# Optimization experiments

Hardware: AMD Instinct MI355X
Metric: run time of the kernel (lower is better)

The kernel has to match this reference:

```python
import jax, jax.numpy as jnp
import numpy as np

ENC_DIM, DEC_DIM, ATT_DIM = 2048, 512, 512

def setup_inputs() -> dict:
    key = jax.random.key(0)
    ks = jax.random.split(key, 8)
    s_enc = 1.0 / np.sqrt(ENC_DIM)
    s_dec = 1.0 / np.sqrt(DEC_DIM)
    s_att = 1.0 / np.sqrt(ATT_DIM)
    return {
        "encoder_out": jax.random.normal(ks[0], (256, 196, ENC_DIM), jnp.float32),
        "decoder_hidden": jax.random.normal(ks[1], (256, DEC_DIM), jnp.float32),
        "W_enc": jax.random.uniform(ks[2], (ENC_DIM, ATT_DIM), jnp.float32, -s_enc, s_enc),
        "b_enc": jax.random.uniform(ks[3], (ATT_DIM,), jnp.float32, -s_enc, s_enc),
        "W_dec": jax.random.uniform(ks[4], (DEC_DIM, ATT_DIM), jnp.float32, -s_dec, s_dec),
        "b_dec": jax.random.uniform(ks[5], (ATT_DIM,), jnp.float32, -s_dec, s_dec),
        "W_att": jax.random.uniform(ks[6], (ATT_DIM, 1), jnp.float32, -s_att, s_att),
        "b_att": jax.random.uniform(ks[7], (1,), jnp.float32, -s_att, s_att),
    }

def reference(encoder_out, decoder_hidden, W_enc, b_enc, W_dec, b_dec, W_att, b_att):
    # att1: (B, P, A); att2: (B, 1, A)
    att1 = jnp.einsum('bpe,ea->bpa', encoder_out, W_enc) + b_enc
    att2 = (decoder_hidden @ W_dec + b_dec)[:, None, :]
    # scalar score per pixel: (B, P)
    e = (jax.nn.relu(att1 + att2) @ W_att)[..., 0] + b_att[0]
    alpha = jax.nn.softmax(e, axis=-1)  # softmax over pixels
    z = jnp.einsum('bpe,bp->be', encoder_out, alpha)
    return (z, alpha)
```

## Files before the change

### kernel.cpp

```cpp
#include <hip/hip_runtime.h>
#include <hip/hip_bf16.h>

#define ENC_DIM 2048
#define DEC_DIM 512
#define ATT_DIM 512
#define NB 256
#define NP 196
#define M_TOT (NB * NP)
#define BM 128
#define BK 32
#define NSTEP (ENC_DIM / BK)

typedef __attribute__((ext_vector_type(8))) short short8;
typedef __attribute__((ext_vector_type(4))) float f32x4;

__device__ __forceinline__ short8 cvt8v(f32x4 x, f32x4 y) {
    union { short8 v; __hip_bfloat16 h[8]; } u;
    u.h[0] = __float2bfloat16(x[0]);
    u.h[1] = __float2bfloat16(x[1]);
    u.h[2] = __float2bfloat16(x[2]);
    u.h[3] = __float2bfloat16(x[3]);
    u.h[4] = __float2bfloat16(y[0]);
    u.h[5] = __float2bfloat16(y[1]);
    u.h[6] = __float2bfloat16(y[2]);
    u.h[7] = __float2bfloat16(y[3]);
    return u.v;
}

__global__ __launch_bounds__(256) void prep_kernel(const float* __restrict__ W,
                                                   __hip_bfloat16* __restrict__ Btt,
                                                   const float* __restrict__ dec,
                                                   const float* __restrict__ W_dec,
                                                   const float* __restrict__ b_dec,
                                                   const float* __restrict__ b_enc,
                                                   float* __restrict__ att2f) {
    __shared__ float ds[DEC_DIM];
    if (blockIdx.x < 512) {
        const int gid = blockIdx.x * 256 + threadIdx.x;
        const int s   = gid >> 11;
        const int u   = gid & 2047;
        const int fr  = u >> 6;
        const int kg  = (u >> 4) & 3;
        const int l15 = u & 15;
        const int col = fr * 16 + l15;
        const int k0  = s * 32 + kg * 8;
        union { short8 v; __hip_bfloat16 h[8]; } x;
        #pragma unroll
        for (int i = 0; i < 8; ++i)
            x.h[i] = __float2bfloat16(W[(size_t)(k0 + i) * ATT_DIM + col]);
        *(short8*)((short*)Btt + (size_t)gid * 8) = x.v;
    } else {
        const int b = blockIdx.x - 512;
        const int t = threadIdx.x;
        ds[t]       = dec[(size_t)b * DEC_DIM + t];
        ds[t + 256] = dec[(size_t)b * DEC_DIM + t + 256];
        __syncthreads();
        #pragma unroll
        for (int j = 0; j < 2; ++j) {
            const int n = t + j * 256;
            float s = 0.f;
            #pragma unroll 8
            for (int k = 0; k < DEC_DIM; ++k)
                s += ds[k] * W_dec[(size_t)k * ATT_DIM + n];
            att2f[(size_t)b * ATT_DIM + n] = s + b_dec[n] + b_enc[n];
        }
    }
}

__global__ __launch_bounds__(512, 2) void e_kernel(const float* __restrict__ enc,
                                                   const short* __restrict__ Btt,
                                                   const float* __restrict__ att2f,
                                                   const float* __restrict__ W_att,
                                                   float* __restrict__ e_part) {
    __shared__ __attribute__((aligned(16))) short As[2][4096];
    __shared__ float ebuf[8][128];

    const int tid  = threadIdx.x;
    const int lane = tid & 63;
    const int wv   = tid >> 6;
    const int l15  = lane & 15;
    const int kg   = lane >> 4;

    const int bid = blockIdx.x;
    const int g   = bid >> 4;
    const int r   = bid & 15;
    const int nh  = r >> 3;
    const int mt  = g * 8 + (r & 7);
    const int M0  = mt * BM;
    const int N0  = nh * 256;

    const int srow = tid >> 2;
    const int sc   = tid & 3;
    const float* asrc = enc + (size_t)(M0 + srow) * ENC_DIM + sc * 8;
    const int awr = (srow >> 4) * 512 + sc * 128 + (srow & 15) * 8;

    const short* pBb = Btt + (nh * 16 + wv * 2) * 512 + kg * 128 + l15 * 8;

    f32x4 acc[8][2];
    #pragma unroll
    for (int i = 0; i < 8; ++i) {
        acc[i][0] = (f32x4){0.f, 0.f, 0.f, 0.f};
        acc[i][1] = (f32x4){0.f, 0.f, 0.f, 0.f};
    }

#define MFMA_STEP(BUF, B0, B1)                                                           \
    {                                                                                    \
        const short* Ab = &As[BUF][0];                                                   \
        _Pragma("unroll")                                                                \
        for (int mf = 0; mf < 8; ++mf) {                                                 \
            const short8 a = *(const short8*)&Ab[mf * 512 + lane * 8];                   \
            acc[mf][0] = __builtin_amdgcn_mfma_f32_16x16x32_bf16(a, B0, acc[mf][0], 0, 0, 0); \
            acc[mf][1] = __builtin_amdgcn_mfma_f32_16x16x32_bf16(a, B1, acc[mf][1], 0, 0, 0); \
        }                                                                                \
    }

    {
        f32x4 lo = *(const f32x4*)asrc;
        f32x4 hi = *(const f32x4*)(asrc + 4);
        *(short8*)&As[0][awr] = cvt8v(lo, hi);
    }
    f32x4 avPa = *(const f32x4*)(asrc + BK);
    f32x4 avPb = *(const f32x4*)(asrc + BK + 4);
    short8 c0 = *(const short8*)(pBb);
    short8 c1 = *(const short8*)(pBb + 512);
    short8 n0, n1;
    asm volatile("s_waitcnt lgkmcnt(0)" ::: "memory");
    __builtin_amdgcn_s_barrier();

    for (int s = 0; s < NSTEP; s += 2) {
        {
            const short* p1 = pBb + (size_t)(s + 1) * 16384;
            n0 = *(const short8*)(p1);
            n1 = *(const short8*)(p1 + 512);
            f32x4 avNa = *(const f32x4*)(asrc + (size_t)((s + 2) & 63) * BK);
            f32x4 avNb = *(const f32x4*)(asrc + (size_t)((s + 2) & 63) * BK + 4);
            __builtin_amdgcn_sched_barrier(0);
            __builtin_amdgcn_s_setprio(1);
            MFMA_STEP(0, c0, c1)
            __builtin_amdgcn_s_setprio(0);
            *(short8*)&As[1][awr] = cvt8v(avPa, avPb);
            avPa = avNa; avPb = avNb;
            asm volatile("s_waitcnt lgkmcnt(0)" ::: "memory");
            __builtin_amdgcn_s_barrier();
        }
        {
            const short* p2 = pBb + (size_t)((s + 2) & 63) * 16384;
            c0 = *(const short8*)(p2);
            c1 = *(const short8*)(p2 + 512);
            f32x4 avNa = *(const f32x4*)(asrc + (size_t)((s + 3) & 63) * BK);
            f32x4 avNb = *(const f32x4*)(asrc + (size_t)((s + 3) & 63) * BK + 4);
            __builtin_amdgcn_sched_barrier(0);
            __builtin_amdgcn_s_setprio(1);
            MFMA_STEP(1, n0, n1)
            __builtin_amdgcn_s_setprio(0);
            *(short8*)&As[0][awr] = cvt8v(avPa, avPb);
            avPa = avNa; avPb = avNb;
            asm volatile("s_waitcnt lgkmcnt(0)" ::: "memory");
            __builtin_amdgcn_s_barrier();
        }
    }
#undef MFMA_STEP

    float wat[2];
    wat[0] = W_att[N0 + wv * 32 + l15];
    wat[1] = W_att[N0 + wv * 32 + 16 + l15];

    #pragma unroll
    for (int mf = 0; mf < 8; ++mf) {
        #pragma unroll
        for (int rr = 0; rr < 4; ++rr) {
            const int ml = mf * 16 + kg * 4 + rr;
            const int bb = (M0 + ml) / NP;
            const float* arow2 = att2f + (size_t)bb * ATT_DIM + N0 + wv * 32 + l15;
            float sv = fmaxf(acc[mf][0][rr] + arow2[0], 0.f) * wat[0] +
                       fmaxf(acc[mf][1][rr] + arow2[16], 0.f) * wat[1];
            sv += __shfl_xor(sv, 1);
            sv += __shfl_xor(sv, 2);
            sv += __shfl_xor(sv, 4);
            sv += __shfl_xor(sv, 8);
            if (l15 == 0) ebuf[wv][ml] = sv;
        }
    }
    __syncthreads();
    if (tid < 128) {
        float sv = 0.f;
        #pragma unroll
        for (int w = 0; w < 8; ++w) sv += ebuf[w][tid];
        e_part[(size_t)nh * M_TOT + M0 + tid] = sv;
    }
}

__global__ __launch_bounds__(256) void z_kernel(const float* __restrict__ enc,
                                                const float* __restrict__ e_part,
                                                float* __restrict__ z,
                                                float* __restrict__ alpha) {
    const int b  = blockIdx.x;
    const int cb = blockIdx.y;
    const int t  = threadIdx.x;
    __shared__ float al[NP];
    __shared__ float red[4];

    float ev = -1e30f;
    if (t < NP)
        ev = e_part[(size_t)b * NP + t] + e_part[(size_t)M_TOT + b * NP + t];
    float m = ev;
    #pragma unroll
    for (int o = 32; o > 0; o >>= 1) m = fmaxf(m, __shfl_xor(m, o));
    if ((t & 63) == 0) red[t >> 6] = m;
    __syncthreads();
    m = fmaxf(fmaxf(red[0], red[1]), fmaxf(red[2], red[3]));
    __syncthreads();
    float ex = (t < NP) ? __expf(ev - m) : 0.f;
    float s = ex;
    #pragma unroll
    for (int o = 32; o > 0; o >>= 1) s += __shfl_xor(s, o);
    if ((t & 63) == 0) red[t >> 6] = s;
    __syncthreads();
    s = red[0] + red[1] + red[2] + red[3];
    const float a = ex * (1.0f / s);
    if (t < NP) {
        al[t] = a;
        if (cb == 0) alpha[(size_t)b * NP + t] = a;
    }
    __syncthreads();

    const int c0 = cb * 1024 + t * 4;
    const float4* ep = (const float4*)(enc + (size_t)b * NP * ENC_DIM + c0);
    float4 z0 = make_float4(0.f, 0.f, 0.f, 0.f);
    float4 z1 = make_float4(0.f, 0.f, 0.f, 0.f);
    #pragma unroll 4
    for (int p = 0; p < NP; p += 2) {
        const float a0 = al[p];
        const float a1 = al[p + 1];
        const float4 v0 = ep[(size_t)p * (ENC_DIM / 4)];
        const float4 v1 = ep[(size_t)(p + 1) * (ENC_DIM / 4)];
        z0.x += a0 * v0.x; z0.y += a0 * v0.y; z0.z += a0 * v0.z; z0.w += a0 * v0.w;
        z1.x += a1 * v1.x; z1.y += a1 * v1.y; z1.z += a1 * v1.z; z1.w += a1 * v1.w;
    }
    z0.x += z1.x; z0.y += z1.y; z0.z += z1.z; z0.w += z1.w;
    *(float4*)(z + (size_t)b * ENC_DIM + c0) = z0;
}

extern "C" void kernel_launch(void* const* d_in, const int* in_sizes, int n_in,
                              void* d_out, int out_size, void* d_ws, size_t ws_size,
                              hipStream_t stream) {
    const float* enc   = (const float*)d_in[0];
    const float* dec   = (const float*)d_in[1];
    const float* W_enc = (const float*)d_in[2];
    const float* b_enc = (const float*)d_in[3];
    const float* W_dec = (const float*)d_in[4];
    const float* b_dec = (const float*)d_in[5];
    const float* W_att = (const float*)d_in[6];

    float* z     = (float*)d_out;
    float* alpha = z + (size_t)NB * ENC_DIM;

    char* ws = (char*)d_ws;
    __hip_bfloat16* Btt = (__hip_bfloat16*)ws;
    float* att2f        = (float*)(ws + 2 * 1024 * 1024);
    float* e_part       = (float*)(ws + 2 * 1024 * 1024 + 512 * 1024);

    prep_kernel<<<768, 256, 0, stream>>>(W_enc, Btt, dec, W_dec, b_dec, b_enc, att2f);
    e_kernel<<<(M_TOT / BM) * 2, 512, 0, stream>>>(enc, (const short*)Btt, att2f, W_att, e_part);
    z_kernel<<<dim3(NB, 2), 256, 0, stream>>>(enc, e_part, z, alpha);
}
```

Measured before the change: 293.2 us.

## Halve e_kernel M tile to 64 rows with 256 threads and 4 N-fragments per wave

Reshapes the e_kernel GEMM tile from 128 rows with 8 waves (each covering 32 columns) to 64 rows with 4 waves (each covering 64 columns via four MFMA accumulator fragments). Each block now stages half as much of encoder_out per K step, and the grid doubles to 1568 blocks, with occupancy raised to 3 blocks per CU. The aim is better load balancing across CUs and more blocks resident at once. The trade-off is lower reuse of the B (weight) operand per block, so W_enc is reread from global/L2 twice as often, and each thread holds more accumulator registers.

```diff
diff --git a/kernel.cpp b/kernel.cpp
--- a/kernel.cpp
+++ b/kernel.cpp
@@ -7,7 +7,7 @@
 #define NB 256
 #define NP 196
 #define M_TOT (NB * NP)
-#define BM 128
+#define BM 64
 #define BK 32
 #define NSTEP (ENC_DIM / BK)
 
@@ -67,13 +67,13 @@
     }
 }
 
-__global__ __launch_bounds__(512, 2) void e_kernel(const float* __restrict__ enc,
+__global__ __launch_bounds__(256, 3) void e_kernel(const float* __restrict__ enc,
                                                    const short* __restrict__ Btt,
                                                    const float* __restrict__ att2f,
                                                    const float* __restrict__ W_att,
                                                    float* __restrict__ e_part) {
-    __shared__ __attribute__((aligned(16))) short As[2][4096];
-    __shared__ float ebuf[8][128];
+    __shared__ __attribute__((aligned(16))) short As[2][2048];
+    __shared__ float ebuf[4][64];
 
     const int tid  = threadIdx.x;
     const int lane = tid & 63;
@@ -94,23 +94,25 @@
     const float* asrc = enc + (size_t)(M0 + srow) * ENC_DIM + sc * 8;
     const int awr = (srow >> 4) * 512 + sc * 128 + (srow & 15) * 8;
 
-    const short* pBb = Btt + (nh * 16 + wv * 2) * 512 + kg * 128 + l15 * 8;
-
-    f32x4 acc[8][2];
-    #pragma unroll
-    for (int i = 0; i < 8; ++i) {
-        acc[i][0] = (f32x4){0.f, 0.f, 0.f, 0.f};
-        acc[i][1] = (f32x4){0.f, 0.f, 0.f, 0.f};
-    }
-
-#define MFMA_STEP(BUF, B0, B1)                                                           \
+    const short* pBb = Btt + (nh * 16 + wv * 4) * 512 + kg * 128 + l15 * 8;
+
+    f32x4 acc[4][4];
+    #pragma unroll
+    for (int i = 0; i < 4; ++i)
+        #pragma unroll
+        for (int j = 0; j < 4; ++j)
+            acc[i][j] = (f32x4){0.f, 0.f, 0.f, 0.f};
+
+#define MFMA16(BUF, B0, B1, B2, B3)                                                      \
     {                                                                                    \
         const short* Ab = &As[BUF][0];                                                   \
         _Pragma("unroll")                                                                \
-        for (int mf = 0; mf < 8; ++mf) {                                                 \
+        for (int mf = 0; mf < 4; ++mf) {                                                 \
             const short8 a = *(const short8*)&Ab[mf * 512 + lane * 8];                   \
             acc[mf][0] = __builtin_amdgcn_mfma_f32_16x16x32_bf16(a, B0, acc[mf][0], 0, 0, 0); \
             acc[mf][1] = __builtin_amdgcn_mfma_f32_16x16x32_bf16(a, B1, acc[mf][1], 0, 0, 0); \
+            acc[mf][2] = __builtin_amdgcn_mfma_f32_16x16x32_bf16(a, B2, acc[mf][2], 0, 0, 0); \
+            acc[mf][3] = __builtin_amdgcn_mfma_f32_16x16x32_bf16(a, B3, acc[mf][3], 0, 0, 0); \
         }                                                                                \
     }
 
@@ -123,7 +125,9 @@
     f32x4 avPb = *(const f32x4*)(asrc + BK + 4);
     short8 c0 = *(const short8*)(pBb);
     short8 c1 = *(const short8*)(pBb + 512);
-    short8 n0, n1;
+    short8 c2 = *(const short8*)(pBb + 1024);
+    short8 c3 = *(const short8*)(pBb + 1536);
+    short8 n0, n1, n2, n3;
     asm volatile("s_waitcnt lgkmcnt(0)" ::: "memory");
     __builtin_amdgcn_s_barrier();
 
@@ -132,11 +136,13 @@
             const short* p1 = pBb + (size_t)(s + 1) * 16384;
             n0 = *(const short8*)(p1);
             n1 = *(const short8*)(p1 + 512);
+            n2 = *(const short8*)(p1 + 1024);
+            n3 = *(const short8*)(p1 + 1536);
             f32x4 avNa = *(const f32x4*)(asrc + (size_t)((s + 2) & 63) * BK);
             f32x4 avNb = *(const f32x4*)(asrc + (size_t)((s + 2) & 63) * BK + 4);
             __builtin_amdgcn_sched_barrier(0);
             __builtin_amdgcn_s_setprio(1);
-            MFMA_STEP(0, c0, c1)
+            MFMA16(0, c0, c1, c2, c3)
             __builtin_amdgcn_s_setprio(0);
             *(short8*)&As[1][awr] = cvt8v(avPa, avPb);
             avPa = avNa; avPb = avNb;
@@ -147,11 +153,13 @@
             const short* p2 = pBb + (size_t)((s + 2) & 63) * 16384;
             c0 = *(const short8*)(p2);
             c1 = *(const short8*)(p2 + 512);
+            c2 = *(const short8*)(p2 + 1024);
+            c3 = *(const short8*)(p2 + 1536);
             f32x4 avNa = *(const f32x4*)(asrc + (size_t)((s + 3) & 63) * BK);
             f32x4 avNb = *(const f32x4*)(asrc + (size_t)((s + 3) & 63) * BK + 4);
             __builtin_amdgcn_sched_barrier(0);
             __builtin_amdgcn_s_setprio(1);
-            MFMA_STEP(1, n0, n1)
+            MFMA16(1, n0, n1, n2, n3)
             __builtin_amdgcn_s_setprio(0);
             *(short8*)&As[0][awr] = cvt8v(avPa, avPb);
             avPa = avNa; avPb = avNb;
@@ -159,21 +167,25 @@
             __builtin_amdgcn_s_barrier();
         }
     }
-#undef MFMA_STEP
-
-    float wat[2];
-    wat[0] = W_att[N0 + wv * 32 + l15];
-    wat[1] = W_att[N0 + wv * 32 + 16 + l15];
-
-    #pragma unroll
-    for (int mf = 0; mf < 8; ++mf) {
+#undef MFMA16
+
+    float wat[4];
+    #pragma unroll
+    for (int nf = 0; nf < 4; ++nf) wat[nf] = W_att[N0 + wv * 64 + nf * 16 + l15];
+
+    #pragma unroll
+    for (int mf = 0; mf < 4; ++mf) {
         #pragma unroll
         for (int rr = 0; rr < 4; ++rr) {
             const int ml = mf * 16 + kg * 4 + rr;
             const int bb = (M0 + ml) / NP;
-            const float* arow2 = att2f + (size_t)bb * ATT_DIM + N0 + wv * 32 + l15;
-            float sv = fmaxf(acc[mf][0][rr] + arow2[0], 0.f) * wat[0] +
-                       fmaxf(acc[mf][1][rr] + arow2[16], 0.f) * wat[1];
+            const float* arow2 = att2f + (size_t)bb * ATT_DIM + N0 + wv * 64 + l15;
+            float sv = 0.f;
+            #pragma unroll
+            for (int nf = 0; nf < 4; ++nf) {
+                float v = acc[mf][nf][rr] + arow2[nf * 16];
+                sv += fmaxf(v, 0.f) * wat[nf];
+            }
             sv += __shfl_xor(sv, 1);
             sv += __shfl_xor(sv, 2);
             sv += __shfl_xor(sv, 4);
@@ -182,12 +194,9 @@
         }
     }
     __syncthreads();
-    if (tid < 128) {
-        float sv = 0.f;
-        #pragma unroll
-        for (int w = 0; w < 8; ++w) sv += ebuf[w][tid];
-        e_part[(size_t)nh * M_TOT + M0 + tid] = sv;
-    }
+    if (tid < 64)
+        e_part[(size_t)nh * M_TOT + M0 + tid] =
+            ebuf[0][tid] + ebuf[1][tid] + ebuf[2][tid] + ebuf[3][tid];
 }
 
 __global__ __launch_bounds__(256) void z_kernel(const float* __restrict__ enc,
@@ -261,6 +270,6 @@
     float* e_part       = (float*)(ws + 2 * 1024 * 1024 + 512 * 1024);
 
     prep_kernel<<<768, 256, 0, stream>>>(W_enc, Btt, dec, W_dec, b_dec, b_enc, att2f);
-    e_kernel<<<(M_TOT / BM) * 2, 512, 0, stream>>>(enc, (const short*)Btt, att2f, W_att, e_part);
+    e_kernel<<<(M_TOT / BM) * 2, 256, 0, stream>>>(enc, (const short*)Btt, att2f, W_att, e_part);
     z_kernel<<<dim3(NB, 2), 256, 0, stream>>>(enc, e_part, z, alpha);
 }
```

After: 310.5 us. 5.9% more time.
